# Kernel optimization log

Measured on AMD Instinct MI355X. Metric: run time of the kernel, lower is better.

## Reference

```python
import jax, jax.numpy as jnp
import numpy as np

B, S, D = 4, 2048, 1024
H = 8  # hardcoded in AttentionLayer
HD = D // H
FF = 4096
EPS = 1e-5


def _layernorm(x):
    # LayerNorm(hidden_dim, elementwise_affine=False), eps=1e-5
    mu = jnp.mean(x, axis=-1, keepdims=True)
    var = jnp.var(x, axis=-1, keepdims=True)
    return (x - mu) / jnp.sqrt(var + EPS)


def setup_inputs() -> dict:
    key = jax.random.key(0)
    ks = jax.random.split(key, 5)
    scale = 0.02
    return {
        "x": jax.random.normal(ks[0], (B, S, D), dtype=jnp.float32),
        "qkv_proj": jax.random.normal(ks[1], (D, 3 * D), dtype=jnp.float32) * scale,
        "o_proj": jax.random.normal(ks[2], (D, D), dtype=jnp.float32) * scale,
        "ff1": jax.random.normal(ks[3], (D, FF), dtype=jnp.float32) * scale,
        "ff2": jax.random.normal(ks[4], (FF, D), dtype=jnp.float32) * scale,
    }


def reference(x, qkv_proj, o_proj, ff1, ff2):
    b, s, d = x.shape
    # --- attention ---
    qkv = jnp.matmul(x, qkv_proj)                       # [b,s,3d]
    qkv = qkv.reshape(b, s, H, 3 * HD).transpose(0, 2, 1, 3)  # [b,h,s,3hd]
    q, k, v = jnp.split(qkv, 3, axis=-1)                # each [b,h,s,hd]
    logits = jnp.einsum('bhqd,bhkd->bhqk', q, k) / jnp.sqrt(jnp.float32(HD))
    attn = jax.nn.softmax(logits, axis=-1)
    vals = jnp.einsum('bhqk,bhkd->bhqd', attn, v)       # [b,h,s,hd]
    vals = vals.transpose(0, 2, 1, 3).reshape(b, s, d)
    attn_out = jnp.matmul(vals, o_proj)
    # --- residual + norm + FFN + residual + norm ---
    x = _layernorm(x + attn_out)
    ff_out = jnp.matmul(jax.nn.relu(jnp.matmul(x, ff1)), ff2)
    x = _layernorm(x + ff_out)
    return x
```

## Files before the change

### kernel.cpp

```cpp
#include <hip/hip_runtime.h>
#include <hip/hip_bf16.h>


typedef float floatx4 __attribute__((ext_vector_type(4)));
typedef float floatx16 __attribute__((ext_vector_type(16)));
typedef short bf16x8 __attribute__((ext_vector_type(8)));

#define DEVI __device__ __forceinline__

typedef const __attribute__((address_space(1))) unsigned int* gas1_t;
typedef __attribute__((address_space(3))) unsigned int* las3_t;

DEVI void gll16(const void* g, void* l) {
  __builtin_amdgcn_global_load_lds((gas1_t)g, (las3_t)l, 16, 0, 0);
}

DEVI short bfbits(float f) {
  __hip_bfloat16 h = __float2bfloat16(f);
  return *reinterpret_cast<short*>(&h);
}

DEVI unsigned int packbf(float lo, float hi) {
  return __builtin_amdgcn_perm(__float_as_uint(hi) + 0x8000u,
                               __float_as_uint(lo) + 0x8000u,
                               0x07060302u);
}

template<int EPI, int SPLITK>
__global__ __launch_bounds__(256, 4) void gemm_bt(
    const __hip_bfloat16* __restrict__ A,
    const __hip_bfloat16* __restrict__ BT,
    __hip_bfloat16* __restrict__ Cb, __hip_bfloat16* __restrict__ Cb2,
    int M, int N, int K)
{
  __shared__ __hip_bfloat16 As[128 * 64];
  __shared__ __hip_bfloat16 Bs[128 * 64];
  const int tid = threadIdx.x;
  const int wave = tid >> 6, lane = tid & 63;
  const int lane15 = lane & 15, quad = lane >> 4;
  const int row0 = blockIdx.x * 128, col0 = blockIdx.y * 128;
  const int wr = (wave >> 1) * 64, wc = (wave & 1) * 64;
  const int Kh = K / SPLITK;
  const size_t kofs = (SPLITK > 1) ? (size_t)blockIdx.z * Kh : 0;

  floatx4 acc[4][4] = {};

  const int srow = tid >> 3;
  const int sblk = (tid & 7) ^ (srow & 7);
  const __hip_bfloat16* Ag = A + (size_t)(row0 + srow) * K + kofs + sblk * 8;
  const __hip_bfloat16* Bg = BT + (size_t)(col0 + srow) * K + kofs + sblk * 8;
  char* Asl = (char*)As + tid * 16;
  char* Bsl = (char*)Bs + tid * 16;
  const size_t rstep = (size_t)32 * K;

  const int x7 = lane15 & 7;
  for (int k0 = 0; k0 < Kh; k0 += 64) {
    __syncthreads();
#pragma unroll
    for (int p = 0; p < 4; p++) {
      gll16(Ag + k0 + p * rstep, Asl + p * 4096);
      gll16(Bg + k0 + p * rstep, Bsl + p * 4096);
    }
    __syncthreads();
#pragma unroll
    for (int kc = 0; kc < 2; kc++) {
      bf16x8 af[4], bb[4];
#pragma unroll
      for (int t = 0; t < 4; t++) {
        const int r = wr + t * 16 + lane15;
        af[t] = *(const bf16x8*)((const char*)As + r * 128 + (((kc * 4 + quad) ^ x7) << 4));
      }
#pragma unroll
      for (int t = 0; t < 4; t++) {
        const int r = wc + t * 16 + lane15;
        bb[t] = *(const bf16x8*)((const char*)Bs + r * 128 + (((kc * 4 + quad) ^ x7) << 4));
      }
#pragma unroll
      for (int i = 0; i < 4; i++)
#pragma unroll
        for (int j = 0; j < 4; j++)
          acc[i][j] = __builtin_amdgcn_mfma_f32_16x16x32_bf16(af[i], bb[j], acc[i][j], 0, 0, 0);
    }
  }

  __hip_bfloat16* Cp = (SPLITK > 1 && blockIdx.z) ? Cb2 : Cb;
#pragma unroll
  for (int i = 0; i < 4; i++) {
    const int mb = row0 + wr + i * 16 + quad * 4;
#pragma unroll
    for (int j = 0; j < 4; j++) {
      const int n = col0 + wc + j * 16 + lane15;
      const float fac = (EPI == 0 && (((n >> 7) % 3) == 0)) ? 0.12751729f : 1.f;
#pragma unroll
      for (int r = 0; r < 4; r++) {
        const size_t idx = (size_t)(mb + r) * N + n;
        const float v = acc[i][j][r];
        if (EPI == 0) {
          Cb[idx] = __float2bfloat16(v * fac);
        } else if (EPI == 2) {
          Cb[idx] = __float2bfloat16(v > 0.f ? v : 0.f);
        } else {
          Cp[idx] = __float2bfloat16(v);
        }
      }
    }
  }
}

__global__ __launch_bounds__(256, 2) void attn_kernel(
    const __hip_bfloat16* __restrict__ qkv,
    const __hip_bfloat16* __restrict__ Vt,
    __hip_bfloat16* __restrict__ vals)
{
  __shared__ __hip_bfloat16 Ak[128 * 128];
  __shared__ __hip_bfloat16 Bq[128 * 128];

  const int tid = threadIdx.x;
  const int wave = tid >> 6, lane = tid & 63;
  const int l31 = lane & 31, l5 = lane >> 5;
  const int bh = blockIdx.x, qt = blockIdx.y;
  const int b = bh >> 3, h = bh & 7;
  const size_t tokbase = (size_t)b * 2048;

  const int sw8 = ((tid & 15) ^ (tid >> 4)) * 8;
  const int srow = tid >> 4;
  const int srowp = (srow & 3) | ((srow << 1) & 8) | ((srow >> 1) & 4);
  const __hip_bfloat16* qg  = qkv + (tokbase + qt * 128) * 3072 + h * 384 + sw8;
  const __hip_bfloat16* kg0 = qkv + tokbase * 3072 + h * 384 + 128 + sw8;
  const __hip_bfloat16* vg0 = Vt + (size_t)bh * 128 * 2048 + sw8;

#pragma unroll
  for (int rd = 0; rd < 8; rd++)
    gll16(qg + (size_t)(rd * 16 + srow) * 3072, (char*)Bq + rd * 4096 + tid * 16);
  __syncthreads();

  const int rx = l31 & 15;
  bf16x8 qf[8];
  {
    const char* qb = (const char*)Bq + (wave * 32 + l31) * 256;
#pragma unroll
    for (int ks = 0; ks < 8; ks++)
      qf[ks] = *(const bf16x8*)(qb + (((ks * 2 + l5) ^ rx) << 4));
  }
#pragma unroll
  for (int rd = 0; rd < 8; rd++)
    gll16(kg0 + (size_t)(rd * 16 + srowp) * 3072, (char*)Ak + rd * 4096 + tid * 16);
  __syncthreads();

  floatx16 oacc[4] = {};
  float lsum = 0.f;

  for (int kt = 0; kt < 16; kt++) {
    if (kt) __syncthreads();

#pragma unroll
    for (int rd = 0; rd < 8; rd++)
      gll16(vg0 + (size_t)kt * 128 + (size_t)(rd * 16 + srow) * 2048,
            (char*)Bq + rd * 4096 + tid * 16);

    floatx16 sacc[4] = {};
#pragma unroll
    for (int ks = 0; ks < 8; ks++) {
      const int off = ((ks * 2 + l5) ^ rx) << 4;
      const char* kb = (const char*)Ak + l31 * 256 + off;
#pragma unroll
      for (int nt = 0; nt < 4; nt++) {
        const bf16x8 ak = *(const bf16x8*)(kb + nt * 8192);
        sacc[nt] = __builtin_amdgcn_mfma_f32_32x32x16_bf16(ak, qf[ks], sacc[nt], 0, 0, 0);
      }
    }

    bf16x8 pf[8];
#pragma unroll
    for (int c = 0; c < 8; c++) {
      const int nt = c >> 1, bi = (c & 1) * 8;
      const float p0 = exp2f(sacc[nt][bi + 0]);
      const float p1 = exp2f(sacc[nt][bi + 1]);
      const float p2 = exp2f(sacc[nt][bi + 2]);
      const float p3 = exp2f(sacc[nt][bi + 3]);
      const float p4 = exp2f(sacc[nt][bi + 4]);
      const float p5 = exp2f(sacc[nt][bi + 5]);
      const float p6 = exp2f(sacc[nt][bi + 6]);
      const float p7 = exp2f(sacc[nt][bi + 7]);
      lsum += ((p0 + p1) + (p2 + p3)) + ((p4 + p5) + (p6 + p7));
      union { uint4 u; bf16x8 v; } w;
      w.u.x = packbf(p0, p1); w.u.y = packbf(p2, p3);
      w.u.z = packbf(p4, p5); w.u.w = packbf(p6, p7);
      pf[c] = w.v;
    }

    __syncthreads();
    if (kt < 15) {
#pragma unroll
      for (int rd = 0; rd < 8; rd++)
        gll16(kg0 + (size_t)((kt + 1) * 128 + rd * 16 + srowp) * 3072,
              (char*)Ak + rd * 4096 + tid * 16);
    }

#pragma unroll
    for (int ks = 0; ks < 8; ks++) {
      const int off = ((ks * 2 + l5) ^ rx) << 4;
      const char* vb = (const char*)Bq + l31 * 256 + off;
#pragma unroll
      for (int nt = 0; nt < 4; nt++) {
        const bf16x8 av = *(const bf16x8*)(vb + nt * 8192);
        oacc[nt] = __builtin_amdgcn_mfma_f32_32x32x16_bf16(av, pf[ks], oacc[nt], 0, 0, 0);
      }
    }
  }

  lsum += __shfl_xor(lsum, 32);
  const float linv = 1.f / lsum;

  const size_t row = tokbase + (size_t)qt * 128 + wave * 32 + l31;
  __hip_bfloat16* vrow = vals + row * 1024 + h * 128 + 4 * l5;
#pragma unroll
  for (int nt = 0; nt < 4; nt++)
#pragma unroll
    for (int g = 0; g < 4; g++) {
      uint2 pk;
      pk.x = packbf(oacc[nt][g * 4 + 0] * linv, oacc[nt][g * 4 + 1] * linv);
      pk.y = packbf(oacc[nt][g * 4 + 2] * linv, oacc[nt][g * 4 + 3] * linv);
      *(uint2*)(vrow + nt * 32 + g * 8) = pk;
    }
}

__global__ __launch_bounds__(256) void prep_k(
    const float* __restrict__ x, __hip_bfloat16* __restrict__ xb,
    const float* __restrict__ qkvw, __hip_bfloat16* __restrict__ qkvT,
    const float* __restrict__ ow, __hip_bfloat16* __restrict__ oT,
    const float* __restrict__ f1, __hip_bfloat16* __restrict__ f1T,
    const float* __restrict__ f2, __hip_bfloat16* __restrict__ f2T)
{
  const int bid = blockIdx.x;
  if (bid < 8192) {
    const size_t i = (size_t)bid * 256 + threadIdx.x;
    const float4 v = ((const float4*)x)[i];
    short4 sv;
    sv.x = bfbits(v.x); sv.y = bfbits(v.y); sv.z = bfbits(v.z); sv.w = bfbits(v.w);
    ((short4*)xb)[i] = sv;
    return;
  }
  int t = bid - 8192;
  const float* W; __hip_bfloat16* WT; int K, N, nbx;
  if (t < 3072) { W = qkvw; WT = qkvT; K = 1024; N = 3072; nbx = 96; }
  else if (t < 3072 + 1024) { t -= 3072; W = ow; WT = oT; K = 1024; N = 1024; nbx = 32; }
  else if (t < 3072 + 1024 + 4096) { t -= 3072 + 1024; W = f1; WT = f1T; K = 1024; N = 4096; nbx = 128; }
  else { t -= 3072 + 1024 + 4096; W = f2; WT = f2T; K = 4096; N = 1024; nbx = 32; }
  __shared__ float tl[32][33];
  const int tx = threadIdx.x & 31, ty = threadIdx.x >> 5;
  const int n0 = (t % nbx) * 32, k0 = (t / nbx) * 32;
#pragma unroll
  for (int i = 0; i < 4; i++)
    tl[ty + i * 8][tx] = W[(size_t)(k0 + ty + i * 8) * N + n0 + tx];
  __syncthreads();
#pragma unroll
  for (int i = 0; i < 4; i++)
    WT[(size_t)(n0 + ty + i * 8) * K + k0 + tx] = __float2bfloat16(tl[tx][ty + i * 8]);
}

__global__ __launch_bounds__(256) void vtrans_k(const __hip_bfloat16* __restrict__ qkv,
                                                __hip_bfloat16* __restrict__ Vt) {
  __shared__ __hip_bfloat16 t[32][33];
  const int tx = threadIdx.x & 31, ty = threadIdx.x >> 5;
  const int s0 = blockIdx.x * 32, d0 = blockIdx.y * 32, bh = blockIdx.z;
  const int b = bh >> 3, h = bh & 7;
#pragma unroll
  for (int i = 0; i < 4; i++)
    t[ty + i * 8][tx] = qkv[((size_t)b * 2048 + s0 + ty + i * 8) * 3072 + h * 384 + 256 + d0 + tx];
  __syncthreads();
#pragma unroll
  for (int i = 0; i < 4; i++)
    Vt[((size_t)bh * 128 + d0 + ty + i * 8) * 2048 + s0 + tx] = t[tx][ty + i * 8];
}

template<bool FINAL>
__global__ __launch_bounds__(256) void ln_red_k(
    const __hip_bfloat16* __restrict__ p0, const __hip_bfloat16* __restrict__ p1,
    const __hip_bfloat16* __restrict__ res,
    __hip_bfloat16* __restrict__ ob, float* __restrict__ of) {
  const int row = blockIdx.x, tid = threadIdx.x;
  const size_t base = (size_t)row * 1024;
  const short4 a4 = ((const short4*)(p0 + base))[tid];
  const short4 b4 = ((const short4*)(p1 + base))[tid];
  const short4 r4 = ((const short4*)(res + base))[tid];
#define BF(x) __bfloat162float(*(const __hip_bfloat16*)&(x))
  float4 v;
  v.x = BF(a4.x) + BF(b4.x) + BF(r4.x);
  v.y = BF(a4.y) + BF(b4.y) + BF(r4.y);
  v.z = BF(a4.z) + BF(b4.z) + BF(r4.z);
  v.w = BF(a4.w) + BF(b4.w) + BF(r4.w);
#undef BF
  float s = v.x + v.y + v.z + v.w;
  float q = v.x * v.x + v.y * v.y + v.z * v.z + v.w * v.w;
#pragma unroll
  for (int off = 32; off; off >>= 1) { s += __shfl_xor(s, off); q += __shfl_xor(q, off); }
  __shared__ float ss[4], sq[4];
  const int wave = tid >> 6;
  if ((tid & 63) == 0) { ss[wave] = s; sq[wave] = q; }
  __syncthreads();
  s = ss[0] + ss[1] + ss[2] + ss[3];
  q = sq[0] + sq[1] + sq[2] + sq[3];
  const float mean = s * (1.f / 1024.f);
  const float var = q * (1.f / 1024.f) - mean * mean;
  const float rstd = rsqrtf(var + 1e-5f);
  float4 o;
  o.x = (v.x - mean) * rstd; o.y = (v.y - mean) * rstd;
  o.z = (v.z - mean) * rstd; o.w = (v.w - mean) * rstd;
  if (FINAL) {
    ((float4*)(of + base))[tid] = o;
  } else {
    short4 sv;
    sv.x = bfbits(o.x); sv.y = bfbits(o.y); sv.z = bfbits(o.z); sv.w = bfbits(o.w);
    ((short4*)(ob + base))[tid] = sv;
  }
}

extern "C" void kernel_launch(void* const* d_in, const int* in_sizes, int n_in,
                              void* d_out, int out_size, void* d_ws, size_t ws_size,
                              hipStream_t stream) {
  const float* x    = (const float*)d_in[0];
  const float* qkvw = (const float*)d_in[1];
  const float* ow   = (const float*)d_in[2];
  const float* f1   = (const float*)d_in[3];
  const float* f2   = (const float*)d_in[4];
  float* out = (float*)d_out;

  char* ws = (char*)d_ws;
  const size_t MB = 1024 * 1024;
  __hip_bfloat16* xb   = (__hip_bfloat16*)(ws);
  __hip_bfloat16* vals = (__hip_bfloat16*)(ws + 16 * MB);
  __hip_bfloat16* P1f  = (__hip_bfloat16*)(ws + 16 * MB);
  __hip_bfloat16* qkvT = (__hip_bfloat16*)(ws + 32 * MB);
  __hip_bfloat16* oT   = (__hip_bfloat16*)(ws + 38 * MB);
  __hip_bfloat16* f1T  = (__hip_bfloat16*)(ws + 40 * MB);
  __hip_bfloat16* f2T  = (__hip_bfloat16*)(ws + 48 * MB);
  __hip_bfloat16* qkvb = (__hip_bfloat16*)(ws + 56 * MB);
  __hip_bfloat16* P0o  = (__hip_bfloat16*)(ws + 56 * MB);
  __hip_bfloat16* P1o  = (__hip_bfloat16*)(ws + 72 * MB);
  __hip_bfloat16* hmid = (__hip_bfloat16*)(ws + 56 * MB);
  __hip_bfloat16* Vt   = (__hip_bfloat16*)(ws + 104 * MB);
  __hip_bfloat16* x1b  = (__hip_bfloat16*)(ws + 120 * MB);
  __hip_bfloat16* P0f  = (__hip_bfloat16*)(ws + 136 * MB);
  (void)in_sizes; (void)n_in; (void)out_size; (void)ws_size;

  prep_k<<<20480, 256, 0, stream>>>(x, xb, qkvw, qkvT, ow, oT, f1, f1T, f2, f2T);
  gemm_bt<0, 1><<<dim3(64, 24, 1), 256, 0, stream>>>(xb, qkvT, qkvb, nullptr,
                                                     8192, 3072, 1024);
  vtrans_k<<<dim3(64, 4, 32), 256, 0, stream>>>(qkvb, Vt);
  attn_kernel<<<dim3(32, 16), 256, 0, stream>>>(qkvb, Vt, vals);
  gemm_bt<4, 2><<<dim3(64, 8, 2), 256, 0, stream>>>(vals, oT, P0o, P1o,
                                                    8192, 1024, 1024);
  ln_red_k<false><<<8192, 256, 0, stream>>>(P0o, P1o, xb, x1b, nullptr);
  gemm_bt<2, 1><<<dim3(64, 32, 1), 256, 0, stream>>>(x1b, f1T, hmid, nullptr,
                                                     8192, 4096, 1024);
  gemm_bt<4, 2><<<dim3(64, 8, 2), 256, 0, stream>>>(hmid, f2T, P0f, P1f,
                                                    8192, 1024, 4096);
  ln_red_k<true><<<8192, 256, 0, stream>>>(P0f, P1f, x1b, nullptr, out);
}
```

Measured before the change: 456.0 us.

## Replace GEMM with 256x256 tile double-buffered pipelined kernel, add setprio and hw bf16 pack

Replaces the 128x128 single-buffered GEMM with a 512-thread 256x256 tile kernel. The new kernel double-buffers LDS and issues global-to-LDS loads for later K tiles while the current tile's MFMAs run, using explicit waitcnt and barriers. MFMA sections are raised with s_setprio in both the GEMM and attention kernels, and the manual bf16 packing is replaced by the v_cvt_pk_bf16_f32 instruction. The goal is more data reuse per tile and less load latency exposed between barriers. The trade-off is 128KB of LDS per block, fewer blocks in flight, and fragile hand-written vmcnt accounting.

New measurement: 454.2 us. No clear change (-0.4%).

```diff
diff --git a/kernel.cpp b/kernel.cpp
--- a/kernel.cpp
+++ b/kernel.cpp
@@ -20,76 +20,123 @@
   return *reinterpret_cast<short*>(&h);
 }
 
-DEVI unsigned int packbf(float lo, float hi) {
-  return __builtin_amdgcn_perm(__float_as_uint(hi) + 0x8000u,
-                               __float_as_uint(lo) + 0x8000u,
-                               0x07060302u);
+DEVI unsigned int cvtpk(float lo, float hi) {
+  unsigned int r;
+  asm("v_cvt_pk_bf16_f32 %0, %1, %2" : "=v"(r) : "v"(lo), "v"(hi));
+  return r;
 }
 
 template<int EPI, int SPLITK>
-__global__ __launch_bounds__(256, 4) void gemm_bt(
+__global__ __launch_bounds__(512, 2) void gemm256(
     const __hip_bfloat16* __restrict__ A,
     const __hip_bfloat16* __restrict__ BT,
     __hip_bfloat16* __restrict__ Cb, __hip_bfloat16* __restrict__ Cb2,
     int M, int N, int K)
 {
-  __shared__ __hip_bfloat16 As[128 * 64];
-  __shared__ __hip_bfloat16 Bs[128 * 64];
+  __shared__ __align__(16) char lds[131072];
   const int tid = threadIdx.x;
   const int wave = tid >> 6, lane = tid & 63;
   const int lane15 = lane & 15, quad = lane >> 4;
-  const int row0 = blockIdx.x * 128, col0 = blockIdx.y * 128;
-  const int wr = (wave >> 1) * 64, wc = (wave & 1) * 64;
+  const int wm = wave >> 2, wn = wave & 3;
+  const int row0 = blockIdx.x * 256, col0 = blockIdx.y * 256;
   const int Kh = K / SPLITK;
   const size_t kofs = (SPLITK > 1) ? (size_t)blockIdx.z * Kh : 0;
-
-  floatx4 acc[4][4] = {};
+  const int NT = Kh >> 6;
+
+  floatx4 acc[8][4] = {};
 
   const int srow = tid >> 3;
   const int sblk = (tid & 7) ^ (srow & 7);
   const __hip_bfloat16* Ag = A + (size_t)(row0 + srow) * K + kofs + sblk * 8;
   const __hip_bfloat16* Bg = BT + (size_t)(col0 + srow) * K + kofs + sblk * 8;
-  char* Asl = (char*)As + tid * 16;
-  char* Bsl = (char*)Bs + tid * 16;
-  const size_t rstep = (size_t)32 * K;
+
+  auto stA = [&](int h, int p, int kt, int bf_) {
+    gll16(Ag + (size_t)(p * 128 + h * 64) * (size_t)K + (size_t)kt * 64,
+          lds + ((h << 1) + bf_) * 16384 + p * 8192 + (tid << 4));
+  };
+  auto stB = [&](int h, int q, int kt, int bf_) {
+    gll16(Bg + (size_t)(h * 128 + q * 64) * (size_t)K + (size_t)kt * 64,
+          lds + 65536 + ((h << 1) + bf_) * 16384 + q * 8192 + (tid << 4));
+  };
 
   const int x7 = lane15 & 7;
-  for (int k0 = 0; k0 < Kh; k0 += 64) {
-    __syncthreads();
-#pragma unroll
-    for (int p = 0; p < 4; p++) {
-      gll16(Ag + k0 + p * rstep, Asl + p * 4096);
-      gll16(Bg + k0 + p * rstep, Bsl + p * 4096);
-    }
-    __syncthreads();
-#pragma unroll
-    for (int kc = 0; kc < 2; kc++) {
-      bf16x8 af[4], bb[4];
-#pragma unroll
-      for (int t = 0; t < 4; t++) {
-        const int r = wr + t * 16 + lane15;
-        af[t] = *(const bf16x8*)((const char*)As + r * 128 + (((kc * 4 + quad) ^ x7) << 4));
+  const int ck0 = (quad ^ x7) << 4;
+  const int ck1 = ((4 + quad) ^ x7) << 4;
+  const int aoff = (wm * 64 + lane15) * 128;
+  const int boff = ((wn & 1) * 64 + lane15) * 128;
+  const int bhalf = wn >> 1;
+
+  stA(0, 0, 0, 0); stA(0, 1, 0, 0);
+  stA(1, 0, 0, 0); stA(1, 1, 0, 0);
+  stB(0, 0, 0, 0); stB(0, 1, 0, 0); stB(1, 0, 0, 0); stB(1, 1, 0, 0);
+  stA(0, 0, 1, 1); stA(0, 1, 1, 1);
+  stB(0, 0, 1, 1); stB(0, 1, 1, 1); stB(1, 0, 1, 1); stB(1, 1, 1, 1);
+  asm volatile("s_waitcnt vmcnt(6)" ::: "memory");
+  asm volatile("s_barrier" ::: "memory");
+
+  for (int t = 0; t < NT; ++t) {
+    const int cb = t & 1, nb = cb ^ 1;
+    const char* As0 = lds + cb * 16384 + aoff;
+    const char* As1 = lds + (2 + cb) * 16384 + aoff;
+    const char* Bs_ = lds + 65536 + ((bhalf << 1) + cb) * 16384 + boff;
+
+    bf16x8 af[4][2], bq[4][2];
+#pragma unroll
+    for (int i = 0; i < 4; i++) {
+      af[i][0] = *(const bf16x8*)(As0 + i * 2048 + ck0);
+      af[i][1] = *(const bf16x8*)(As0 + i * 2048 + ck1);
+    }
+#pragma unroll
+    for (int j = 0; j < 4; j++) {
+      bq[j][0] = *(const bf16x8*)(Bs_ + j * 2048 + ck0);
+      bq[j][1] = *(const bf16x8*)(Bs_ + j * 2048 + ck1);
+    }
+    if (t + 1 < NT) { stA(1, 0, t + 1, nb); stA(1, 1, t + 1, nb); }
+    asm volatile("s_barrier" ::: "memory");
+    __builtin_amdgcn_s_setprio(1);
+#pragma unroll
+    for (int i = 0; i < 4; i++)
+#pragma unroll
+      for (int j = 0; j < 4; j++) {
+        acc[i][j] = __builtin_amdgcn_mfma_f32_16x16x32_bf16(af[i][0], bq[j][0], acc[i][j], 0, 0, 0);
+        acc[i][j] = __builtin_amdgcn_mfma_f32_16x16x32_bf16(af[i][1], bq[j][1], acc[i][j], 0, 0, 0);
       }
-#pragma unroll
-      for (int t = 0; t < 4; t++) {
-        const int r = wc + t * 16 + lane15;
-        bb[t] = *(const bf16x8*)((const char*)Bs + r * 128 + (((kc * 4 + quad) ^ x7) << 4));
+    __builtin_amdgcn_s_setprio(0);
+    asm volatile("s_barrier" ::: "memory");
+
+#pragma unroll
+    for (int i = 0; i < 4; i++) {
+      af[i][0] = *(const bf16x8*)(As1 + i * 2048 + ck0);
+      af[i][1] = *(const bf16x8*)(As1 + i * 2048 + ck1);
+    }
+    if (t + 2 < NT) {
+      stA(0, 0, t + 2, cb); stA(0, 1, t + 2, cb);
+      stB(0, 0, t + 2, cb); stB(0, 1, t + 2, cb);
+      stB(1, 0, t + 2, cb); stB(1, 1, t + 2, cb);
+      asm volatile("s_waitcnt vmcnt(6)" ::: "memory");
+    } else if (t + 1 < NT) {
+      asm volatile("s_waitcnt vmcnt(0)" ::: "memory");
+    }
+    asm volatile("s_barrier" ::: "memory");
+    __builtin_amdgcn_s_setprio(1);
+#pragma unroll
+    for (int i = 0; i < 4; i++)
+#pragma unroll
+      for (int j = 0; j < 4; j++) {
+        acc[4 + i][j] = __builtin_amdgcn_mfma_f32_16x16x32_bf16(af[i][0], bq[j][0], acc[4 + i][j], 0, 0, 0);
+        acc[4 + i][j] = __builtin_amdgcn_mfma_f32_16x16x32_bf16(af[i][1], bq[j][1], acc[4 + i][j], 0, 0, 0);
       }
-#pragma unroll
-      for (int i = 0; i < 4; i++)
-#pragma unroll
-        for (int j = 0; j < 4; j++)
-          acc[i][j] = __builtin_amdgcn_mfma_f32_16x16x32_bf16(af[i], bb[j], acc[i][j], 0, 0, 0);
-    }
+    __builtin_amdgcn_s_setprio(0);
+    asm volatile("s_barrier" ::: "memory");
   }
 
   __hip_bfloat16* Cp = (SPLITK > 1 && blockIdx.z) ? Cb2 : Cb;
 #pragma unroll
-  for (int i = 0; i < 4; i++) {
-    const int mb = row0 + wr + i * 16 + quad * 4;
+  for (int i = 0; i < 8; i++) {
+    const int mb = row0 + wm * 128 + i * 16 + quad * 4;
 #pragma unroll
     for (int j = 0; j < 4; j++) {
-      const int n = col0 + wc + j * 16 + lane15;
+      const int n = col0 + wn * 64 + j * 16 + lane15;
       const float fac = (EPI == 0 && (((n >> 7) % 3) == 0)) ? 0.12751729f : 1.f;
 #pragma unroll
       for (int r = 0; r < 4; r++) {
@@ -159,6 +206,7 @@
             (char*)Bq + rd * 4096 + tid * 16);
 
     floatx16 sacc[4] = {};
+    __builtin_amdgcn_s_setprio(1);
 #pragma unroll
     for (int ks = 0; ks < 8; ks++) {
       const int off = ((ks * 2 + l5) ^ rx) << 4;
@@ -169,6 +217,7 @@
         sacc[nt] = __builtin_amdgcn_mfma_f32_32x32x16_bf16(ak, qf[ks], sacc[nt], 0, 0, 0);
       }
     }
+    __builtin_amdgcn_s_setprio(0);
 
     bf16x8 pf[8];
 #pragma unroll
@@ -184,8 +233,8 @@
       const float p7 = exp2f(sacc[nt][bi + 7]);
       lsum += ((p0 + p1) + (p2 + p3)) + ((p4 + p5) + (p6 + p7));
       union { uint4 u; bf16x8 v; } w;
-      w.u.x = packbf(p0, p1); w.u.y = packbf(p2, p3);
-      w.u.z = packbf(p4, p5); w.u.w = packbf(p6, p7);
+      w.u.x = cvtpk(p0, p1); w.u.y = cvtpk(p2, p3);
+      w.u.z = cvtpk(p4, p5); w.u.w = cvtpk(p6, p7);
       pf[c] = w.v;
     }
 
@@ -197,6 +246,7 @@
               (char*)Ak + rd * 4096 + tid * 16);
     }
 
+    __builtin_amdgcn_s_setprio(1);
 #pragma unroll
     for (int ks = 0; ks < 8; ks++) {
       const int off = ((ks * 2 + l5) ^ rx) << 4;
@@ -207,6 +257,7 @@
         oacc[nt] = __builtin_amdgcn_mfma_f32_32x32x16_bf16(av, pf[ks], oacc[nt], 0, 0, 0);
       }
     }
+    __builtin_amdgcn_s_setprio(0);
   }
 
   lsum += __shfl_xor(lsum, 32);
@@ -219,8 +270,8 @@
 #pragma unroll
     for (int g = 0; g < 4; g++) {
       uint2 pk;
-      pk.x = packbf(oacc[nt][g * 4 + 0] * linv, oacc[nt][g * 4 + 1] * linv);
-      pk.y = packbf(oacc[nt][g * 4 + 2] * linv, oacc[nt][g * 4 + 3] * linv);
+      pk.x = cvtpk(oacc[nt][g * 4 + 0] * linv, oacc[nt][g * 4 + 1] * linv);
+      pk.y = cvtpk(oacc[nt][g * 4 + 2] * linv, oacc[nt][g * 4 + 3] * linv);
       *(uint2*)(vrow + nt * 32 + g * 8) = pk;
     }
 }
@@ -345,16 +396,16 @@
   (void)in_sizes; (void)n_in; (void)out_size; (void)ws_size;
 
   prep_k<<<20480, 256, 0, stream>>>(x, xb, qkvw, qkvT, ow, oT, f1, f1T, f2, f2T);
-  gemm_bt<0, 1><<<dim3(64, 24, 1), 256, 0, stream>>>(xb, qkvT, qkvb, nullptr,
+  gemm256<0, 1><<<dim3(32, 12, 1), 512, 0, stream>>>(xb, qkvT, qkvb, nullptr,
                                                      8192, 3072, 1024);
   vtrans_k<<<dim3(64, 4, 32), 256, 0, stream>>>(qkvb, Vt);
   attn_kernel<<<dim3(32, 16), 256, 0, stream>>>(qkvb, Vt, vals);
-  gemm_bt<4, 2><<<dim3(64, 8, 2), 256, 0, stream>>>(vals, oT, P0o, P1o,
+  gemm256<4, 2><<<dim3(32, 4, 2), 512, 0, stream>>>(vals, oT, P0o, P1o,
                                                     8192, 1024, 1024);
   ln_red_k<false><<<8192, 256, 0, stream>>>(P0o, P1o, xb, x1b, nullptr);
-  gemm_bt<2, 1><<<dim3(64, 32, 1), 256, 0, stream>>>(x1b, f1T, hmid, nullptr,
+  gemm256<2, 1><<<dim3(32, 16, 1), 512, 0, stream>>>(x1b, f1T, hmid, nullptr,
                                                      8192, 4096, 1024);
-  gemm_bt<4, 2><<<dim3(64, 8, 2), 256, 0, stream>>>(hmid, f2T, P0f, P1f,
+  gemm256<4, 2><<<dim3(32, 4, 2), 512, 0, stream>>>(hmid, f2T, P0f, P1f,
                                                     8192, 1024, 4096);
   ln_red_k<true><<<8192, 256, 0, stream>>>(P0f, P1f, x1b, nullptr, out);
 }
```
